# Optimization experiments

Measured on AMD Instinct MI355X. Metric: run time of the kernel, lower is better.

## Reference

```python
import jax, jax.numpy as jnp
import numpy as np

C_IN = 512      # backbone feature dim (din)
CORR = 256      # cfg.SIAMESE.NUM_CHANNELS_FOR_CORRELATION
EXPAND = 64     # expand_factor
N_ANCH = 9      # 3 scales x 3 ratios
KH = 7          # template spatial size
H = W = 32      # target feature map size
N_T = 2         # number of templates
BN_EPS = 1e-5


def _conv(x, w, b=None, pad=0, groups=1):
    out = jax.lax.conv_general_dilated(
        x, w, window_strides=(1, 1), padding=[(pad, pad), (pad, pad)],
        dimension_numbers=('NCHW', 'OIHW', 'NCHW'), feature_group_count=groups)
    if b is not None:
        out = out + b[None, :, None, None]
    return out


def setup_inputs() -> dict:
    key = jax.random.key(0)
    ks = jax.random.split(key, 10)
    return {
        'target_feat': jax.random.normal(ks[0], (1, C_IN, H, W), jnp.float32),
        'template_feat': jax.random.normal(ks[1], (N_T, C_IN, KH, KH), jnp.float32),
        'w_target': jax.random.normal(ks[2], (CORR, C_IN, 3, 3), jnp.float32) * 0.01,
        'b_target': jnp.zeros((CORR,), jnp.float32),
        'bn_gamma': jnp.ones((CORR,), jnp.float32),
        'bn_beta': jnp.zeros((CORR,), jnp.float32),
        'bn_mean': jax.random.normal(ks[3], (CORR,), jnp.float32) * 0.1,
        'bn_var': jax.random.uniform(ks[4], (CORR,), jnp.float32, 0.5, 1.5),
        'w_template': jax.random.normal(ks[5], (CORR * EXPAND, C_IN, 3, 3), jnp.float32) * 0.01,
        'b_template': jnp.zeros((CORR * EXPAND,), jnp.float32),
        'w_merge_cls': jax.random.normal(ks[6], (CORR,), jnp.float32) * 0.01,
        'corr_bias': jnp.zeros((EXPAND, 1, 1), jnp.float32),
        'w_cls': jax.random.normal(ks[7], (2 * N_ANCH, EXPAND, 1, 1), jnp.float32) * 0.01,
        'b_cls': jnp.zeros((2 * N_ANCH,), jnp.float32),
        'w_box': jax.random.normal(ks[8], (4 * N_ANCH, EXPAND, 1, 1), jnp.float32) * 0.001,
        'b_box': jnp.zeros((4 * N_ANCH,), jnp.float32),
    }


def reference(target_feat, template_feat, w_target, b_target, bn_gamma, bn_beta,
              bn_mean, bn_var, w_template, b_template, w_merge_cls, corr_bias,
              w_cls, b_cls, w_box, b_box):
    N = template_feat.shape[0]
    Hh, Ww = target_feat.shape[2], target_feat.shape[3]
    # RPN_Conv_target (3x3, pad 1) + BatchNorm (eval mode, running stats)
    t = _conv(target_feat, w_target, b_target, pad=1)               # (1, CORR, H, W)
    scale = (bn_gamma / jnp.sqrt(bn_var + BN_EPS))[None, :, None, None]
    t = (t - bn_mean[None, :, None, None]) * scale + bn_beta[None, :, None, None]
    # RPN_Conv_template (3x3, pad 1) on template features
    z = _conv(template_feat, w_template, b_template, pad=1)          # (N, CORR*EXPAND, kh, kw)
    kh, kw = z.shape[2], z.shape[3]
    # depth-wise cross correlation: kernel (N*EXPAND*CORR, 1, kh, kw), groups=CORR
    kern = z.reshape(N * EXPAND * CORR, 1, kh, kw)
    out = 0.1 * _conv(t, kern, pad=(kh - 1) // 2, groups=CORR)       # (1, N*EXPAND*CORR, H, W)
    out = out.reshape(N * EXPAND, CORR, Hh, Ww)
    # conv_merge_1x1_cls: 1x1 conv CORR -> 1, no bias
    out = jnp.einsum('nchw,c->nhw', out, w_merge_cls)                # (N*EXPAND, H, W)
    rpn_feat = out.reshape(N, EXPAND, Hh, Ww) + corr_bias[None]      # (N, 64, H, W)
    # cls / bbox heads (1x1 convs)
    cls = _conv(rpn_feat, w_cls, b_cls)                              # (N, 18, H, W)
    box = _conv(rpn_feat, w_box, b_box)                              # (N, 36, H, W)
    nc = cls.shape[1]
    # reshape to (N, 2, A*H, W), softmax over dim 1, reshape back
    prob = jax.nn.softmax(cls.reshape(N, 2, (nc // 2) * Hh, Ww), axis=1)
    prob = prob.reshape(N, nc, Hh, Ww)
    return prob, box
```

## Files before the change

kernel.cpp:

```cpp
#include <hip/hip_runtime.h>
#include <math.h>


#define WS_TFP 0
#define WS_TP  591872
#define WS_BF  980992
#define WS_WFP 981120
#define WS_Z2P 3340416
#define WS_MRG 3741824
#define WS_CVP 3872896
#define WFP_SLAB 589824

typedef float f4u __attribute__((ext_vector_type(4), aligned(4)));
typedef float f4a __attribute__((ext_vector_type(4)));

#define FMA4A(accv, ww, vv) \
  accv.x = fmaf(ww, (vv).x, accv.x); accv.y = fmaf(ww, (vv).y, accv.y); \
  accv.z = fmaf(ww, (vv).z, accv.z); accv.w = fmaf(ww, (vv).w, accv.w)

#define NTL(p) __builtin_nontemporal_load((const f4a*)(p))

__global__ __launch_bounds__(256) void k_fold(
    const float* __restrict__ wtpl,
    const float* __restrict__ wm,
    float* ws)
{
  const int g = blockIdx.x >> 2, sub = blockIdx.x & 3;
  const int tid = threadIdx.x;
  __shared__ float wS[32];
  if (tid < 32) wS[tid] = wm[(g & 1) * 128 + sub * 32 + tid];
  __syncthreads();
  const float* base = wtpl + (size_t)(g * 128 + sub * 32) * 4608;
  const int c0 = tid * 4;
  const int c4 = 4096 + (tid & 127) * 4;
  const bool tail = (tid < 128);
  f4a a0 = {0.f, 0.f, 0.f, 0.f}, a1 = a0, a2 = a0, a3 = a0, a4 = a0;
  #pragma unroll 2
  for (int r = 0; r < 32; r++) {
    const float* row = base + (size_t)r * 4608;
    const f4a v0 = NTL(row + c0);
    const f4a v1 = NTL(row + c0 + 1024);
    const f4a v2 = NTL(row + c0 + 2048);
    const f4a v3 = NTL(row + c0 + 3072);
    f4a v4 = {0.f, 0.f, 0.f, 0.f};
    if (tail) v4 = NTL(row + c4);
    const float w = wS[r];
    FMA4A(a0, w, v0); FMA4A(a1, w, v1); FMA4A(a2, w, v2);
    FMA4A(a3, w, v3); FMA4A(a4, w, v4);
  }
  float* wp = ws + WS_WFP + (size_t)sub * WFP_SLAB + (size_t)g * 4608;
  *(f4a*)(wp + c0) = a0;
  *(f4a*)(wp + c0 + 1024) = a1;
  *(f4a*)(wp + c0 + 2048) = a2;
  *(f4a*)(wp + c0 + 3072) = a3;
  if (tail) *(f4a*)(wp + c4) = a4;
}

__global__ __launch_bounds__(256) void k0_prep(
    const float* __restrict__ tfeat,
    const float* __restrict__ wm,
    const float* __restrict__ btpl,
    float* ws)
{
  const int N0 = 591872, N2 = 389120;
  const int total = N0 + N2;
  for (int idx = blockIdx.x * 256 + threadIdx.x; idx < total + 128; idx += gridDim.x * 256) {
    if (idx < N0) {
      int ci = idx / 1156, r = idx % 1156;
      int yy = r / 34, xx = r % 34;
      float v = 0.f;
      if (yy >= 1 && yy <= 32 && xx >= 1 && xx <= 32)
        v = tfeat[ci * 1024 + (yy - 1) * 32 + (xx - 1)];
      ws[WS_TFP + idx] = v;
    } else if (idx < total) {
      ws[WS_TP + (idx - N0)] = 0.f;
    } else {
      const int eh = idx - total;
      const int e = eh >> 1, h = eh & 1;
      const float* wmp = wm + h * 128;
      const float* bp = btpl + e * 256 + h * 128;
      float s = 0.f;
      for (int cl = 0; cl < 128; cl++) s = fmaf(wmp[cl], bp[cl], s);
      ws[WS_BF + eh] = s;
    }
  }
}

__global__ __launch_bounds__(256) void k_conv(
    const float* __restrict__ wtgt,
    float* ws)
{
  const int bid = blockIdx.x;
  const int coblk = bid >> 7, pxblk = (bid >> 3) & 15, ks = bid & 7;
  const int tid = threadIdx.x;
  const int ksub = tid >> 7, sub = tid & 127;
  const int cog = sub >> 5, pxg = sub & 31;
  const int row = pxg >> 4, x0 = (pxg & 15) * 2;
  const int y = pxblk * 2 + row;
  const int co0 = coblk * 16 + cog * 4;
  const int ci0 = ks * 64 + ksub * 32;
  const float* tfp = ws + WS_TFP;

  float acc[4][2] = {{0.f, 0.f}, {0.f, 0.f}, {0.f, 0.f}, {0.f, 0.f}};
  for (int i = 0; i < 32; i++) {
    const int ci = ci0 + i;
    const float* tin = tfp + (size_t)ci * 1156 + y * 34 + x0;
    const f4u p0 = *(const f4u*)(tin);
    const f4u p1 = *(const f4u*)(tin + 34);
    const f4u p2 = *(const f4u*)(tin + 68);
    #pragma unroll
    for (int c = 0; c < 4; c++) {
      const float* wr = wtgt + (size_t)(co0 + c) * 4608 + ci * 9;
      const f4u wa = *(const f4u*)(wr);
      const f4u wb = *(const f4u*)(wr + 4);
      const float w8 = wr[8];
      acc[c][0] += wa.x * p0.x + wa.y * p0.y + wa.z * p0.z
                 + wa.w * p1.x + wb.x * p1.y + wb.y * p1.z
                 + wb.z * p2.x + wb.w * p2.y + w8 * p2.z;
      acc[c][1] += wa.x * p0.y + wa.y * p0.z + wa.z * p0.w
                 + wa.w * p1.y + wb.x * p1.z + wb.y * p1.w
                 + wb.z * p2.y + wb.w * p2.z + w8 * p2.w;
    }
  }
  float* cvp = ws + WS_CVP + (size_t)(ks * 2 + ksub) * 262144;
  #pragma unroll
  for (int c = 0; c < 4; c++) {
    cvp[(co0 + c) * 1024 + y * 32 + x0 + 0] = acc[c][0];
    cvp[(co0 + c) * 1024 + y * 32 + x0 + 1] = acc[c][1];
  }
}

__global__ __launch_bounds__(256) void k_cred(
    const float* __restrict__ btgt,
    const float* __restrict__ gamma, const float* __restrict__ beta,
    const float* __restrict__ mean, const float* __restrict__ var,
    float* ws)
{
  const int co = blockIdx.x;
  const int tid = threadIdx.x;
  const float sc = gamma[co] * rsqrtf(var[co] + 1e-5f);
  const float off = btgt[co] - mean[co];
  const float bt = beta[co];
  const float* cvp = ws + WS_CVP + (size_t)co * 1024;
  float* tP = ws + WS_TP;
  #pragma unroll
  for (int k = 0; k < 4; k++) {
    const int j = k * 256 + tid;
    float s = 0.f;
    #pragma unroll
    for (int sl = 0; sl < 16; sl++) s += cvp[(size_t)sl * 262144 + j];
    const float t = ((s + off) * sc + bt) * 0.1f;
    const int yy = j >> 5, xx = j & 31;
    tP[co * 1520 + (yy + 3) * 40 + (xx + 3)] = t;
  }
}

__global__ __launch_bounds__(256) void k2_z2(
    const float* __restrict__ zfeat,
    float* ws)
{
  __shared__ float Tl[50][144];
  const int tid = threadIdx.x;
  const int n = blockIdx.x >> 5, kc = blockIdx.x & 31;
  const int ci0 = kc * 16;
  for (int idx = tid; idx < 7200; idx += 256) {
    const int uv = idx / 144, kk = idx % 144;
    float v = 0.f;
    if (uv < 49) {
      const int u = uv / 7, vv = uv % 7;
      const int ci = ci0 + kk / 9, pq = kk % 9;
      const int p = pq / 3, q = pq % 3;
      const int yy = u + p - 1, xx = vv + q - 1;
      if (yy >= 0 && yy < 7 && xx >= 0 && xx < 7)
        v = zfeat[n * 25088 + ci * 49 + yy * 7 + xx];
    }
    Tl[uv][kk] = v;
  }
  __syncthreads();
  const int ehq = tid & 31, uvg = tid >> 5;
  const int eh0 = ehq * 4;
  const int uv0 = (uvg == 0) ? 0 : uvg * 6 + 1;
  const float* wfp = ws + WS_WFP;
  float4 acc[7];
  #pragma unroll
  for (int i = 0; i < 7; i++) acc[i] = make_float4(0.f, 0.f, 0.f, 0.f);
  for (int g = 0; g < 36; g++) {
    const int koff = ci0 * 9 + g * 4;
    f4a wvE[4];
    #pragma unroll
    for (int e = 0; e < 4; e++) {
      const float* pe = wfp + (size_t)(eh0 + e) * 4608 + koff;
      f4a a = *(const f4a*)(pe);
      a += *(const f4a*)(pe + WFP_SLAB);
      f4a b2 = *(const f4a*)(pe + 2 * WFP_SLAB);
      b2 += *(const f4a*)(pe + 3 * WFP_SLAB);
      wvE[e] = a + b2;
    }
    #pragma unroll
    for (int uu = 0; uu < 7; uu++) {
      const float4 t4 = *(const float4*)(&Tl[uv0 + uu][g * 4]);
      acc[uu].x = fmaf(t4.x, wvE[0].x, fmaf(t4.y, wvE[0].y, fmaf(t4.z, wvE[0].z, fmaf(t4.w, wvE[0].w, acc[uu].x))));
      acc[uu].y = fmaf(t4.x, wvE[1].x, fmaf(t4.y, wvE[1].y, fmaf(t4.z, wvE[1].z, fmaf(t4.w, wvE[1].w, acc[uu].y))));
      acc[uu].z = fmaf(t4.x, wvE[2].x, fmaf(t4.y, wvE[2].y, fmaf(t4.z, wvE[2].z, fmaf(t4.w, wvE[2].w, acc[uu].z))));
      acc[uu].w = fmaf(t4.x, wvE[3].x, fmaf(t4.y, wvE[3].y, fmaf(t4.z, wvE[3].z, fmaf(t4.w, wvE[3].w, acc[uu].w))));
    }
  }
  float* z2p = ws + WS_Z2P;
  #pragma unroll
  for (int uu = 0; uu < 7; uu++) {
    const int uv = uv0 + uu;
    if (uv <= 48)
      *(float4*)(z2p + ((size_t)((n * 32 + kc) * 49 + uv)) * 128 + eh0) = acc[uu];
  }
}

__global__ __launch_bounds__(128) void k3_merged(float* ws)
{
  __shared__ float Z2s[16][7][8];
  const int tid = threadIdx.x;
  const int bid = blockIdx.x;
  const int n = bid >> 7, rest = bid & 127;
  const int ec = rest >> 4, hq = rest & 15;
  const int c0 = ec * 16, h0 = hq * 2;
  const float* z2p = ws + WS_Z2P;
  const float* bf = ws + WS_BF;
  for (int idx = tid; idx < 784; idx += 128) {
    const int cl = idx & 15, uv = idx >> 4;
    float s = bf[c0 + cl];
    const float* p = z2p + (size_t)(n * 1568 + uv) * 128 + (c0 + cl);
    #pragma unroll 8
    for (int kc = 0; kc < 32; kc++) s += p[(size_t)kc * 6272];
    Z2s[cl][uv / 7][uv % 7] = s;
  }
  for (int idx = tid; idx < 112; idx += 128)
    Z2s[idx / 7][idx % 7][7] = 0.f;
  __syncthreads();

  const int e = tid >> 4, row = (tid >> 3) & 1, wq = tid & 7;
  const int w0 = wq * 4;
  const float* tP = ws + WS_TP;
  float acc[4] = {0.f, 0.f, 0.f, 0.f};
  #pragma unroll
  for (int h128 = 0; h128 < 2; h128++) {
    const int cl = 2 * e + h128;
    const float* tc = tP + (size_t)(128 * n + c0 + cl) * 1520;
    #pragma unroll
    for (int u = 0; u < 7; u++) {
      const float* trow = tc + (h0 + row + u) * 40 + w0;
      float tw[12];
      *(float4*)&tw[0] = *(const float4*)(trow);
      *(float4*)&tw[4] = *(const float4*)(trow + 4);
      *(float4*)&tw[8] = *(const float4*)(trow + 8);
      float z[8];
      *(float4*)&z[0] = *(const float4*)&Z2s[cl][u][0];
      *(float4*)&z[4] = *(const float4*)&Z2s[cl][u][4];
      #pragma unroll
      for (int px = 0; px < 4; px++)
        #pragma unroll
        for (int v = 0; v < 8; v++)
          acc[px] = fmaf(z[v], tw[px + v], acc[px]);
    }
  }
  float* mrg = ws + WS_MRG;
  *(float4*)(mrg + (size_t)(((n * 64 + ec * 8 + e) * 32) + h0 + row) * 32 + w0) =
      make_float4(acc[0], acc[1], acc[2], acc[3]);
}

__global__ __launch_bounds__(256) void k4_heads(
    const float* __restrict__ cb,
    const float* __restrict__ wcls, const float* __restrict__ bcls,
    const float* __restrict__ wbox, const float* __restrict__ bbox,
    float* ws, float* __restrict__ out)
{
  __shared__ float mrg_l[32][66];
  __shared__ float wcb_l[54][64];
  __shared__ float bias_l[54];
  __shared__ float logits[18][32];
  const int tid = threadIdx.x;
  const int n = blockIdx.x >> 5, h = blockIdx.x & 31;
  const float* mrg = ws + WS_MRG;
  for (int idx = tid; idx < 2048; idx += 256) {
    const int e = idx >> 5, w = idx & 31;
    mrg_l[w][e] = mrg[(size_t)(((n * 64 + e) * 32) + h) * 32 + w] + cb[e];
  }
  for (int idx = tid; idx < 3456; idx += 256) {
    const int ch = idx >> 6, e = idx & 63;
    wcb_l[ch][e] = (ch < 18) ? wcls[ch * 64 + e] : wbox[(ch - 18) * 64 + e];
  }
  if (tid < 54) bias_l[tid] = (tid < 18) ? bcls[tid] : bbox[tid - 18];
  __syncthreads();

  const int w = tid & 31, chg = tid >> 5;
  const int cnt = (chg < 6) ? 7 : 6;
  float acc[7] = {0.f, 0.f, 0.f, 0.f, 0.f, 0.f, 0.f};
  for (int e2 = 0; e2 < 32; e2++) {
    const float2 m2 = *(const float2*)&mrg_l[w][e2 * 2];
    #pragma unroll
    for (int i = 0; i < 7; i++) {
      if (i < cnt) {
        const int ch = chg + 8 * i;
        const float2 wv = *(const float2*)&wcb_l[ch][e2 * 2];
        acc[i] = fmaf(m2.x, wv.x, acc[i]);
        acc[i] = fmaf(m2.y, wv.y, acc[i]);
      }
    }
  }
  #pragma unroll
  for (int i = 0; i < 7; i++) {
    if (i < cnt) {
      const int ch = chg + 8 * i;
      const float v = acc[i] + bias_l[ch];
      if (ch < 18) logits[ch][w] = v;
      else out[36864 + n * 36864 + (ch - 18) * 1024 + h * 32 + w] = v;
    }
  }
  __syncthreads();
  for (int idx = tid; idx < 576; idx += 256) {
    const int ch = idx >> 5, w2 = idx & 31;
    const float a = logits[ch][w2];
    const float b = logits[(ch + 9) % 18][w2];
    const float m = fmaxf(a, b);
    const float ea = expf(a - m), eb = expf(b - m);
    out[n * 18432 + ch * 1024 + h * 32 + w2] = ea / (ea + eb);
  }
}

extern "C" void kernel_launch(void* const* d_in, const int* in_sizes, int n_in,
                              void* d_out, int out_size, void* d_ws, size_t ws_size,
                              hipStream_t stream) {
  (void)in_sizes; (void)n_in; (void)out_size; (void)ws_size;
  const float* target_feat   = (const float*)d_in[0];
  const float* template_feat = (const float*)d_in[1];
  const float* w_target      = (const float*)d_in[2];
  const float* b_target      = (const float*)d_in[3];
  const float* bn_gamma      = (const float*)d_in[4];
  const float* bn_beta       = (const float*)d_in[5];
  const float* bn_mean       = (const float*)d_in[6];
  const float* bn_var        = (const float*)d_in[7];
  const float* w_template    = (const float*)d_in[8];
  const float* b_template    = (const float*)d_in[9];
  const float* w_merge       = (const float*)d_in[10];
  const float* corr_bias     = (const float*)d_in[11];
  const float* w_cls         = (const float*)d_in[12];
  const float* b_cls         = (const float*)d_in[13];
  const float* w_box         = (const float*)d_in[14];
  const float* b_box         = (const float*)d_in[15];
  float* ws = (float*)d_ws;
  float* out = (float*)d_out;

  hipLaunchKernelGGL(k_fold, dim3(512), dim3(256), 0, stream,
                     w_template, w_merge, ws);
  hipLaunchKernelGGL(k0_prep, dim3(2048), dim3(256), 0, stream,
                     target_feat, w_merge, b_template, ws);
  hipLaunchKernelGGL(k_conv, dim3(2048), dim3(256), 0, stream,
                     w_target, ws);
  hipLaunchKernelGGL(k_cred, dim3(256), dim3(256), 0, stream,
                     b_target, bn_gamma, bn_beta, bn_mean, bn_var, ws);
  hipLaunchKernelGGL(k2_z2, dim3(64), dim3(256), 0, stream,
                     template_feat, ws);
  hipLaunchKernelGGL(k3_merged, dim3(256), dim3(128), 0, stream, ws);
  hipLaunchKernelGGL(k4_heads, dim3(64), dim3(256), 0, stream,
                     corr_bias, w_cls, b_cls, w_box, b_box, ws, out);
}
```

Before: 273.0 us.

## Fold template weights with async global-to-LDS double-buffered pipeline, drop partial slabs

```diff
diff --git a/kernel.cpp b/kernel.cpp
--- a/kernel.cpp
+++ b/kernel.cpp
@@ -1,59 +1,67 @@
 #include <hip/hip_runtime.h>
 #include <math.h>
+#include <stdint.h>
 
 
 #define WS_TFP 0
 #define WS_TP  591872
 #define WS_BF  980992
 #define WS_WFP 981120
-#define WS_Z2P 3340416
-#define WS_MRG 3741824
-#define WS_CVP 3872896
-#define WFP_SLAB 589824
+#define WS_Z2P 1570944
+#define WS_MRG 1972352
+#define WS_CVP 2103424
 
 typedef float f4u __attribute__((ext_vector_type(4), aligned(4)));
 typedef float f4a __attribute__((ext_vector_type(4)));
-
-#define FMA4A(accv, ww, vv) \
-  accv.x = fmaf(ww, (vv).x, accv.x); accv.y = fmaf(ww, (vv).y, accv.y); \
-  accv.z = fmaf(ww, (vv).z, accv.z); accv.w = fmaf(ww, (vv).w, accv.w)
-
-#define NTL(p) __builtin_nontemporal_load((const f4a*)(p))
 
 __global__ __launch_bounds__(256) void k_fold(
     const float* __restrict__ wtpl,
     const float* __restrict__ wm,
     float* ws)
 {
-  const int g = blockIdx.x >> 2, sub = blockIdx.x & 3;
-  const int tid = threadIdx.x;
-  __shared__ float wS[32];
-  if (tid < 32) wS[tid] = wm[(g & 1) * 128 + sub * 32 + tid];
-  __syncthreads();
-  const float* base = wtpl + (size_t)(g * 128 + sub * 32) * 4608;
-  const int c0 = tid * 4;
-  const int c4 = 4096 + (tid & 127) * 4;
-  const bool tail = (tid < 128);
-  f4a a0 = {0.f, 0.f, 0.f, 0.f}, a1 = a0, a2 = a0, a3 = a0, a4 = a0;
-  #pragma unroll 2
-  for (int r = 0; r < 32; r++) {
-    const float* row = base + (size_t)r * 4608;
-    const f4a v0 = NTL(row + c0);
-    const f4a v1 = NTL(row + c0 + 1024);
-    const f4a v2 = NTL(row + c0 + 2048);
-    const f4a v3 = NTL(row + c0 + 3072);
-    f4a v4 = {0.f, 0.f, 0.f, 0.f};
-    if (tail) v4 = NTL(row + c4);
-    const float w = wS[r];
-    FMA4A(a0, w, v0); FMA4A(a1, w, v1); FMA4A(a2, w, v2);
-    FMA4A(a3, w, v3); FMA4A(a4, w, v4);
-  }
-  float* wp = ws + WS_WFP + (size_t)sub * WFP_SLAB + (size_t)g * 4608;
-  *(f4a*)(wp + c0) = a0;
-  *(f4a*)(wp + c0 + 1024) = a1;
-  *(f4a*)(wp + c0 + 2048) = a2;
-  *(f4a*)(wp + c0 + 3072) = a3;
-  if (tail) *(f4a*)(wp + c4) = a4;
+  const int g = blockIdx.x / 9, chunk = blockIdx.x % 9;
+  const int tid = threadIdx.x;
+  const int wid = tid >> 6, lane = tid & 63;
+  __shared__ float st[2][8192];
+  __shared__ float wS[128];
+  if (tid < 128) wS[tid] = wm[(g & 1) * 128 + tid];
+  const float* gbase = wtpl + (size_t)(g * 128) * 4608 + chunk * 512;
+
+  auto issue_stage = [&](int buf, int s) {
+    const float* sb = gbase + (size_t)(s * 16) * 4608;
+    #pragma unroll
+    for (int i = 0; i < 8; i++) {
+      const int call = wid * 8 + i;
+      const int row = call >> 1, half = call & 1;
+      const float* src = sb + (size_t)row * 4608 + half * 256 + lane * 4;
+      float* dst = &st[buf][row * 512 + half * 256];
+      __builtin_amdgcn_global_load_lds((const uint32_t*)src, (uint32_t*)dst,
+                                       16, 0, 0);
+    }
+  };
+
+  issue_stage(0, 0);
+  float accx = 0.f, accy = 0.f;
+  for (int s = 0; s < 8; s++) {
+    if (s < 7) {
+      issue_stage((s + 1) & 1, s + 1);
+      asm volatile("s_waitcnt vmcnt(8)" ::: "memory");
+    } else {
+      asm volatile("s_waitcnt vmcnt(0)" ::: "memory");
+    }
+    __syncthreads();
+    const float* buf = st[s & 1];
+    #pragma unroll
+    for (int r = 0; r < 16; r++) {
+      const float wgt = wS[s * 16 + r];
+      accx = fmaf(wgt, buf[r * 512 + tid], accx);
+      accy = fmaf(wgt, buf[r * 512 + 256 + tid], accy);
+    }
+    __syncthreads();
+  }
+  float* wp = ws + WS_WFP + (size_t)g * 4608 + chunk * 512;
+  wp[tid] = accx;
+  wp[tid + 256] = accy;
 }
 
 __global__ __launch_bounds__(256) void k0_prep(
@@ -190,11 +198,7 @@
     #pragma unroll
     for (int e = 0; e < 4; e++) {
       const float* pe = wfp + (size_t)(eh0 + e) * 4608 + koff;
-      f4a a = *(const f4a*)(pe);
-      a += *(const f4a*)(pe + WFP_SLAB);
-      f4a b2 = *(const f4a*)(pe + 2 * WFP_SLAB);
-      b2 += *(const f4a*)(pe + 3 * WFP_SLAB);
-      wvE[e] = a + b2;
+      wvE[e] = *(const f4a*)(pe);
     }
     #pragma unroll
     for (int uu = 0; uu < 7; uu++) {
@@ -348,7 +352,7 @@
   float* ws = (float*)d_ws;
   float* out = (float*)d_out;
 
-  hipLaunchKernelGGL(k_fold, dim3(512), dim3(256), 0, stream,
+  hipLaunchKernelGGL(k_fold, dim3(1152), dim3(256), 0, stream,
                      w_template, w_merge, ws);
   hipLaunchKernelGGL(k0_prep, dim3(2048), dim3(256), 0, stream,
                      target_feat, w_merge, b_template, ws);
```

After: 231.9 us. -15.1%, faster.
